# Optimization experiments

Measured on AMD Instinct MI355X. Metric: run time of the kernel, lower is better.

## Reference

```python
import jax, jax.numpy as jnp
import numpy as np

EPS = 1e-12  # torch F.normalize default eps (clamp_min)

def _l2norm(v, axis):
    n = jnp.sqrt(jnp.sum(v * v, axis=axis, keepdims=True))
    return v / jnp.maximum(n, EPS)

def setup_inputs() -> dict:
    key = jax.random.key(0)
    k1, k2, k3 = jax.random.split(key, 3)
    N, D, H, W, K = 64, 128, 64, 64, 32
    x = jax.random.normal(k1, (N, D, H, W), dtype=jnp.float32)
    conv_w = jax.random.normal(k2, (K, D), dtype=jnp.float32)  # 1x1 conv weight, no bias
    centroids = jax.random.uniform(k3, (K, D), dtype=jnp.float32)
    return {"x": x, "conv_w": conv_w, "centroids": centroids}

def reference(x, conv_w, centroids):
    N, D, H, W = x.shape
    K = conv_w.shape[0]
    # descriptor-wise L2 normalization over channel dim
    x = _l2norm(x, axis=1)
    xf = x.reshape(N, D, H * W)                      # [N, D, P]
    # 1x1 conv == per-pixel linear: [K,D] @ [N,D,P] -> [N,K,P]
    logits = jnp.einsum('kd,ndp->nkp', conv_w, xf)
    soft_assign = jax.nn.softmax(logits, axis=1)     # softmax over clusters
    # vlad[n,k,d] = sum_p a[n,k,p]*(x[n,d,p] - c[k,d])
    #            = (a @ x^T)[n,k,d] - (sum_p a)[n,k] * c[k,d]
    agg = jnp.einsum('nkp,ndp->nkd', soft_assign, xf)
    asum = jnp.sum(soft_assign, axis=2)              # [N, K]
    vlad = agg - asum[:, :, None] * centroids[None]  # [N, K, D]
    vlad = _l2norm(vlad, axis=2)                     # intra-normalization
    vlad = vlad.reshape(N, K * D)
    vlad = _l2norm(vlad, axis=1)                     # global L2 norm
    return vlad
```

## Files before the change

### kernel.cpp

```cpp
#include <hip/hip_runtime.h>
#include <math.h>

#define N_IMG 64
#define D_CH  128
#define P_PIX 4096
#define K_CL  32
#define S_SPL 8
#define P_BLK (P_PIX / S_SPL)
#define TP    32
#define N_TILE (P_BLK / TP)

typedef __attribute__((ext_vector_type(8))) short bf16x8;
typedef __attribute__((ext_vector_type(4))) float f32x4;

#define MFMA(a, b, c) __builtin_amdgcn_mfma_f32_16x16x32_bf16(a, b, c, 0, 0, 0)

#define BAR() do {                                            \
    asm volatile("s_waitcnt lgkmcnt(0)" ::: "memory");        \
    __builtin_amdgcn_s_barrier();                             \
} while (0)

static __device__ __forceinline__ void split4t(float a, float b, float c, float d,
                                               ushort4 &h, ushort4 &l) {
    unsigned ua = __float_as_uint(a), ub = __float_as_uint(b);
    unsigned uc = __float_as_uint(c), ud = __float_as_uint(d);
    h.x = (ushort)(ua >> 16); h.y = (ushort)(ub >> 16);
    h.z = (ushort)(uc >> 16); h.w = (ushort)(ud >> 16);
    float ra = a - __uint_as_float(ua & 0xffff0000u);
    float rb = b - __uint_as_float(ub & 0xffff0000u);
    float rc = c - __uint_as_float(uc & 0xffff0000u);
    float rd = d - __uint_as_float(ud & 0xffff0000u);
    l.x = (ushort)(__float_as_uint(ra) >> 16);
    l.y = (ushort)(__float_as_uint(rb) >> 16);
    l.z = (ushort)(__float_as_uint(rc) >> 16);
    l.w = (ushort)(__float_as_uint(rd) >> 16);
}

__global__ __launch_bounds__(256)
void netvlad_main(const float* __restrict__ x, const float* __restrict__ w,
                  float* __restrict__ aggp, float* __restrict__ asump)
{
    __shared__ __align__(16) ushort xTh[32 * 136], xTl[32 * 136];
    __shared__ __align__(16) ushort xDh[128 * 40], xDl[128 * 40];
    __shared__ __align__(16) ushort aph[32 * 40],  apl[32 * 40];
    __shared__ __align__(16) float  xch[4][64][4];
    __shared__ float pbuf[4][32];
    __shared__ float asw[4][16];

    const int tid = threadIdx.x;
    const int n   = blockIdx.x >> 3;
    const int ps  = blockIdx.x & 7;

    const int l   = tid & 63;
    const int wid = tid >> 6;
    const int q   = l >> 4;
    const int ln  = l & 15;
    const int mt  = wid >> 1;
    const int nt  = wid & 1;

    bf16x8 wh[4], wl[4];
    #pragma unroll
    for (int kk = 0; kk < 4; ++kk) {
        const float* wp = w + (nt * 16 + ln) * D_CH + kk * 32 + 8 * q;
        float4 wa = *(const float4*)wp;
        float4 wb = *(const float4*)(wp + 4);
        ushort4 h1, l1, h2, l2;
        split4t(wa.x, wa.y, wa.z, wa.w, h1, l1);
        split4t(wb.x, wb.y, wb.z, wb.w, h2, l2);
        wh[kk][0] = (short)h1.x; wh[kk][1] = (short)h1.y; wh[kk][2] = (short)h1.z; wh[kk][3] = (short)h1.w;
        wh[kk][4] = (short)h2.x; wh[kk][5] = (short)h2.y; wh[kk][6] = (short)h2.z; wh[kk][7] = (short)h2.w;
        wl[kk][0] = (short)l1.x; wl[kk][1] = (short)l1.y; wl[kk][2] = (short)l1.z; wl[kk][3] = (short)l1.w;
        wl[kk][4] = (short)l2.x; wl[kk][5] = (short)l2.y; wl[kk][6] = (short)l2.z; wl[kk][7] = (short)l2.w;
    }

    f32x4 acc2[2][2];
    #pragma unroll
    for (int a = 0; a < 2; ++a)
        #pragma unroll
        for (int b = 0; b < 2; ++b)
            acc2[a][b] = (f32x4){0.f, 0.f, 0.f, 0.f};
    float asacc = 0.0f;

    const float* xin = x + (size_t)n * D_CH * P_PIX + ps * P_BLK;

    const int pT    = tid & 31;
    const int dbase = (tid >> 5) * 16;

    float4 xv[4];
    float  tv[16];
    {
        const float* xt = xin;
        #pragma unroll
        for (int it = 0; it < 4; ++it) {
            int d = it * 32 + (tid >> 3);
            xv[it] = *(const float4*)(xt + d * P_PIX + 4 * (tid & 7));
        }
        #pragma unroll
        for (int j = 0; j < 16; ++j)
            tv[j] = xt[(size_t)(dbase + j) * P_PIX + pT];
    }

    for (int t = 0; t < N_TILE; ++t) {
        #pragma unroll
        for (int it = 0; it < 4; ++it) {
            int d = it * 32 + (tid >> 3);
            ushort4 h, lo;
            split4t(xv[it].x, xv[it].y, xv[it].z, xv[it].w, h, lo);
            *(ushort4*)&xDh[d * 40 + 4 * (tid & 7)] = h;
            *(ushort4*)&xDl[d * 40 + 4 * (tid & 7)] = lo;
        }

        float sq = 0.f;
        #pragma unroll
        for (int c = 0; c < 4; ++c) {
            ushort4 h, lo;
            split4t(tv[4*c+0], tv[4*c+1], tv[4*c+2], tv[4*c+3], h, lo);
            *(ushort4*)&xTh[pT * 136 + dbase + 4 * c] = h;
            *(ushort4*)&xTl[pT * 136 + dbase + 4 * c] = lo;
            sq += tv[4*c+0]*tv[4*c+0] + tv[4*c+1]*tv[4*c+1]
                + tv[4*c+2]*tv[4*c+2] + tv[4*c+3]*tv[4*c+3];
        }
        sq += __shfl_xor(sq, 32);
        if (l < 32) pbuf[wid][pT] = sq;

        if (t + 1 < N_TILE) {
            const float* xt2 = xin + (t + 1) * TP;
            #pragma unroll
            for (int it = 0; it < 4; ++it) {
                int d = it * 32 + (tid >> 3);
                xv[it] = *(const float4*)(xt2 + d * P_PIX + 4 * (tid & 7));
            }
            #pragma unroll
            for (int j = 0; j < 16; ++j)
                tv[j] = xt2[(size_t)(dbase + j) * P_PIX + pT];
        }
        BAR();

        float spx, spy, spz, spw;
        {
            int pp = l & 31;
            int jb = (l >> 5) * 2;
            float vsq = pbuf[jb][pp] + pbuf[jb + 1][pp];
            vsq += __shfl_xor(vsq, 32);
            float sSl = 1.0f / fmaxf(sqrtf(vsq), 1e-12f);
            int p0 = mt * 16 + 4 * q;
            spx = __shfl(sSl, p0 + 0);
            spy = __shfl(sSl, p0 + 1);
            spz = __shfl(sSl, p0 + 2);
            spw = __shfl(sSl, p0 + 3);
        }

        f32x4 acc1 = (f32x4){0.f, 0.f, 0.f, 0.f};
        #pragma unroll
        for (int kk = 0; kk < 4; ++kk) {
            int ia = (mt * 16 + ln) * 136 + kk * 32 + 8 * q;
            bf16x8 Ah = *(const bf16x8*)&xTh[ia];
            bf16x8 Al = *(const bf16x8*)&xTl[ia];
            acc1 = MFMA(Ah, wh[kk], acc1);
            acc1 = MFMA(Ah, wl[kk], acc1);
            acc1 = MFMA(Al, wh[kk], acc1);
        }

        float e[4], s[4];
        e[0] = __builtin_expf(acc1[0] * spx);
        e[1] = __builtin_expf(acc1[1] * spy);
        e[2] = __builtin_expf(acc1[2] * spz);
        e[3] = __builtin_expf(acc1[3] * spw);
        #pragma unroll
        for (int r = 0; r < 4; ++r) {
            s[r] = e[r];
            s[r] += __shfl_xor(s[r], 1);
            s[r] += __shfl_xor(s[r], 2);
            s[r] += __shfl_xor(s[r], 4);
            s[r] += __shfl_xor(s[r], 8);
        }
        *(float4*)&xch[wid][l][0] = make_float4(s[0], s[1], s[2], s[3]);
        BAR();
        {
            float4 po = *(const float4*)&xch[wid ^ 1][l][0];
            float rt[4];
            rt[0] = __builtin_amdgcn_rcpf(s[0] + po.x);
            rt[1] = __builtin_amdgcn_rcpf(s[1] + po.y);
            rt[2] = __builtin_amdgcn_rcpf(s[2] + po.z);
            rt[3] = __builtin_amdgcn_rcpf(s[3] + po.w);
            float sm[4], ap[4];
            #pragma unroll
            for (int r = 0; r < 4; ++r) sm[r] = e[r] * rt[r];
            asacc += sm[0] + sm[1] + sm[2] + sm[3];
            ap[0] = sm[0] * spx; ap[1] = sm[1] * spy;
            ap[2] = sm[2] * spz; ap[3] = sm[3] * spw;
            ushort4 h, lo;
            split4t(ap[0], ap[1], ap[2], ap[3], h, lo);
            int ib = (nt * 16 + ln) * 40 + mt * 16 + 4 * q;
            *(ushort4*)&aph[ib] = h;
            *(ushort4*)&apl[ib] = lo;
        }
        BAR();

        bf16x8 A2h[2], A2l[2], B2h[2], B2l[2];
        #pragma unroll
        for (int m2 = 0; m2 < 2; ++m2) {
            int ia = ((2 * wid + m2) * 16 + ln) * 40 + 8 * q;
            A2h[m2] = *(const bf16x8*)&xDh[ia];
            A2l[m2] = *(const bf16x8*)&xDl[ia];
        }
        #pragma unroll
        for (int n2 = 0; n2 < 2; ++n2) {
            int ib = (n2 * 16 + ln) * 40 + 8 * q;
            B2h[n2] = *(const bf16x8*)&aph[ib];
            B2l[n2] = *(const bf16x8*)&apl[ib];
        }
        #pragma unroll
        for (int m2 = 0; m2 < 2; ++m2)
            #pragma unroll
            for (int n2 = 0; n2 < 2; ++n2) {
                acc2[m2][n2] = MFMA(A2h[m2], B2h[n2], acc2[m2][n2]);
                acc2[m2][n2] = MFMA(A2h[m2], B2l[n2], acc2[m2][n2]);
                acc2[m2][n2] = MFMA(A2l[m2], B2h[n2], acc2[m2][n2]);
            }
        BAR();
    }

    const int base = ((n * S_SPL + ps) * K_CL) * D_CH;
    #pragma unroll
    for (int m2 = 0; m2 < 2; ++m2)
        #pragma unroll
        for (int n2 = 0; n2 < 2; ++n2) {
            int k = n2 * 16 + ln;
            #pragma unroll
            for (int r = 0; r < 4; ++r) {
                int d = (2 * wid + m2) * 16 + 4 * q + r;
                aggp[base + k * D_CH + d] = acc2[m2][n2][r];
            }
        }
    asacc += __shfl_xor(asacc, 16);
    asacc += __shfl_xor(asacc, 32);
    if (l < 16) asw[wid][l] = asacc;
    __syncthreads();
    if (tid < K_CL)
        asump[(n * S_SPL + ps) * K_CL + tid] =
            asw[tid >> 4][tid & 15] + asw[(tid >> 4) + 2][tid & 15];
}

__global__ __launch_bounds__(256)
void netvlad_finish(const float* __restrict__ aggp, const float* __restrict__ asump,
                    const float* __restrict__ cen, float* __restrict__ out)
{
    __shared__ float red[K_CL][8];
    __shared__ float gw[4];
    __shared__ float gss;
    const int tid = threadIdx.x;
    const int n = blockIdx.x;
    const int k = tid >> 3;
    const int d0 = (tid & 7) << 4;

    float v[16];
    #pragma unroll
    for (int i = 0; i < 16; ++i) v[i] = 0.0f;
    float as = 0.0f;
    for (int qq = 0; qq < S_SPL; ++qq) {
        const float* src = aggp + (((n * S_SPL + qq) * K_CL) + k) * D_CH + d0;
        #pragma unroll
        for (int c = 0; c < 4; ++c) {
            float4 t4 = *(const float4*)(src + (c << 2));
            v[4*c+0] += t4.x; v[4*c+1] += t4.y; v[4*c+2] += t4.z; v[4*c+3] += t4.w;
        }
        as += asump[(n * S_SPL + qq) * K_CL + k];
    }
    const float* cp = cen + k * D_CH + d0;
    float ssq = 0.0f;
    #pragma unroll
    for (int c = 0; c < 4; ++c) {
        float4 c4 = *(const float4*)(cp + (c << 2));
        v[4*c+0] -= as * c4.x;
        v[4*c+1] -= as * c4.y;
        v[4*c+2] -= as * c4.z;
        v[4*c+3] -= as * c4.w;
    }
    #pragma unroll
    for (int i = 0; i < 16; ++i) ssq += v[i] * v[i];
    red[k][tid & 7] = ssq;
    __syncthreads();
    float s2 = 0.0f;
    #pragma unroll
    for (int j = 0; j < 8; ++j) s2 += red[k][j];
    const float sc1 = 1.0f / fmaxf(sqrtf(s2), 1e-12f);
    #pragma unroll
    for (int i = 0; i < 16; ++i) v[i] *= sc1;
    float g = ssq * sc1 * sc1;
    #pragma unroll
    for (int off = 1; off < 64; off <<= 1) g += __shfl_xor(g, off);
    if ((tid & 63) == 0) gw[tid >> 6] = g;
    __syncthreads();
    if (tid == 0) gss = 1.0f / fmaxf(sqrtf(gw[0] + gw[1] + gw[2] + gw[3]), 1e-12f);
    __syncthreads();
    const float gsc = gss;
    float* op = out + (size_t)n * (K_CL * D_CH) + k * D_CH + d0;
    #pragma unroll
    for (int c = 0; c < 4; ++c) {
        *(float4*)(op + (c << 2)) =
            make_float4(v[4*c+0]*gsc, v[4*c+1]*gsc, v[4*c+2]*gsc, v[4*c+3]*gsc);
    }
}

extern "C" void kernel_launch(void* const* d_in, const int* in_sizes, int n_in,
                              void* d_out, int out_size, void* d_ws, size_t ws_size,
                              hipStream_t stream)
{
    const float* x   = (const float*)d_in[0];
    const float* w   = (const float*)d_in[1];
    const float* cen = (const float*)d_in[2];
    float* out = (float*)d_out;

    float* aggp  = (float*)d_ws;
    float* asump = aggp + (size_t)N_IMG * S_SPL * K_CL * D_CH;

    netvlad_main<<<N_IMG * S_SPL, 256, 0, stream>>>(x, w, aggp, asump);
    netvlad_finish<<<N_IMG, 256, 0, stream>>>(aggp, asump, cen, out);
}
```

Baseline: 52.47 us.

## Load MFMA operands directly from global memory and double pixel tile size

```diff
diff --git a/kernel.cpp b/kernel.cpp
--- a/kernel.cpp
+++ b/kernel.cpp
@@ -7,8 +7,9 @@
 #define K_CL  32
 #define S_SPL 8
 #define P_BLK (P_PIX / S_SPL)
-#define TP    32
+#define TP    64
 #define N_TILE (P_BLK / TP)
+#define APLD  72
 
 typedef __attribute__((ext_vector_type(8))) short bf16x8;
 typedef __attribute__((ext_vector_type(4))) float f32x4;
@@ -36,16 +37,22 @@
     l.w = (ushort)(__float_as_uint(rd) >> 16);
 }
 
+static __device__ __forceinline__ void split8f(const float f[8], bf16x8 &h, bf16x8 &l) {
+    #pragma unroll
+    for (int i = 0; i < 8; ++i) {
+        unsigned u = __float_as_uint(f[i]);
+        h[i] = (short)(u >> 16);
+        float r = f[i] - __uint_as_float(u & 0xffff0000u);
+        l[i] = (short)(__float_as_uint(r) >> 16);
+    }
+}
+
 __global__ __launch_bounds__(256)
 void netvlad_main(const float* __restrict__ x, const float* __restrict__ w,
                   float* __restrict__ aggp, float* __restrict__ asump)
 {
-    __shared__ __align__(16) ushort xTh[32 * 136], xTl[32 * 136];
-    __shared__ __align__(16) ushort xDh[128 * 40], xDl[128 * 40];
-    __shared__ __align__(16) ushort aph[32 * 40],  apl[32 * 40];
-    __shared__ __align__(16) float  xch[4][64][4];
-    __shared__ float pbuf[4][32];
-    __shared__ float asw[4][16];
+    __shared__ __align__(16) ushort aph[K_CL * APLD], apl[K_CL * APLD];
+    __shared__ float asw[4][32];
 
     const int tid = threadIdx.x;
     const int n   = blockIdx.x >> 3;
@@ -55,23 +62,18 @@
     const int wid = tid >> 6;
     const int q   = l >> 4;
     const int ln  = l & 15;
-    const int mt  = wid >> 1;
-    const int nt  = wid & 1;
-
-    bf16x8 wh[4], wl[4];
-    #pragma unroll
-    for (int kk = 0; kk < 4; ++kk) {
-        const float* wp = w + (nt * 16 + ln) * D_CH + kk * 32 + 8 * q;
-        float4 wa = *(const float4*)wp;
-        float4 wb = *(const float4*)(wp + 4);
-        ushort4 h1, l1, h2, l2;
-        split4t(wa.x, wa.y, wa.z, wa.w, h1, l1);
-        split4t(wb.x, wb.y, wb.z, wb.w, h2, l2);
-        wh[kk][0] = (short)h1.x; wh[kk][1] = (short)h1.y; wh[kk][2] = (short)h1.z; wh[kk][3] = (short)h1.w;
-        wh[kk][4] = (short)h2.x; wh[kk][5] = (short)h2.y; wh[kk][6] = (short)h2.z; wh[kk][7] = (short)h2.w;
-        wl[kk][0] = (short)l1.x; wl[kk][1] = (short)l1.y; wl[kk][2] = (short)l1.z; wl[kk][3] = (short)l1.w;
-        wl[kk][4] = (short)l2.x; wl[kk][5] = (short)l2.y; wl[kk][6] = (short)l2.z; wl[kk][7] = (short)l2.w;
-    }
+
+    bf16x8 wh[2][4], wl[2][4];
+    #pragma unroll
+    for (int n2 = 0; n2 < 2; ++n2)
+        #pragma unroll
+        for (int kk = 0; kk < 4; ++kk) {
+            const float* wp = w + (n2 * 16 + ln) * D_CH + kk * 32 + 8 * q;
+            float fv[8];
+            *(float4*)&fv[0] = *(const float4*)wp;
+            *(float4*)&fv[4] = *(const float4*)(wp + 4);
+            split8f(fv, wh[n2][kk], wl[n2][kk]);
+        }
 
     f32x4 acc2[2][2];
     #pragma unroll
@@ -79,145 +81,116 @@
         #pragma unroll
         for (int b = 0; b < 2; ++b)
             acc2[a][b] = (f32x4){0.f, 0.f, 0.f, 0.f};
-    float asacc = 0.0f;
+    float asacc0 = 0.0f, asacc1 = 0.0f;
 
     const float* xin = x + (size_t)n * D_CH * P_PIX + ps * P_BLK;
-
-    const int pT    = tid & 31;
-    const int dbase = (tid >> 5) * 16;
-
-    float4 xv[4];
-    float  tv[16];
-    {
-        const float* xt = xin;
-        #pragma unroll
-        for (int it = 0; it < 4; ++it) {
-            int d = it * 32 + (tid >> 3);
-            xv[it] = *(const float4*)(xt + d * P_PIX + 4 * (tid & 7));
-        }
-        #pragma unroll
-        for (int j = 0; j < 16; ++j)
-            tv[j] = xt[(size_t)(dbase + j) * P_PIX + pT];
-    }
+    const int base_p = wid * 16 + ln;
 
     for (int t = 0; t < N_TILE; ++t) {
-        #pragma unroll
-        for (int it = 0; it < 4; ++it) {
-            int d = it * 32 + (tid >> 3);
-            ushort4 h, lo;
-            split4t(xv[it].x, xv[it].y, xv[it].z, xv[it].w, h, lo);
-            *(ushort4*)&xDh[d * 40 + 4 * (tid & 7)] = h;
-            *(ushort4*)&xDl[d * 40 + 4 * (tid & 7)] = lo;
-        }
+        const float* xt = xin + t * TP;
+
+        float av[4][8];
+        #pragma unroll
+        for (int kk = 0; kk < 4; ++kk)
+            #pragma unroll
+            for (int j = 0; j < 8; ++j)
+                av[kk][j] = xt[(size_t)(kk * 32 + 8 * q + j) * P_PIX + base_p];
 
         float sq = 0.f;
         #pragma unroll
-        for (int c = 0; c < 4; ++c) {
-            ushort4 h, lo;
-            split4t(tv[4*c+0], tv[4*c+1], tv[4*c+2], tv[4*c+3], h, lo);
-            *(ushort4*)&xTh[pT * 136 + dbase + 4 * c] = h;
-            *(ushort4*)&xTl[pT * 136 + dbase + 4 * c] = lo;
-            sq += tv[4*c+0]*tv[4*c+0] + tv[4*c+1]*tv[4*c+1]
-                + tv[4*c+2]*tv[4*c+2] + tv[4*c+3]*tv[4*c+3];
-        }
+        for (int kk = 0; kk < 4; ++kk)
+            #pragma unroll
+            for (int j = 0; j < 8; ++j)
+                sq += av[kk][j] * av[kk][j];
+        sq += __shfl_xor(sq, 16);
         sq += __shfl_xor(sq, 32);
-        if (l < 32) pbuf[wid][pT] = sq;
-
-        if (t + 1 < N_TILE) {
-            const float* xt2 = xin + (t + 1) * TP;
-            #pragma unroll
-            for (int it = 0; it < 4; ++it) {
-                int d = it * 32 + (tid >> 3);
-                xv[it] = *(const float4*)(xt2 + d * P_PIX + 4 * (tid & 7));
-            }
-            #pragma unroll
-            for (int j = 0; j < 16; ++j)
-                tv[j] = xt2[(size_t)(dbase + j) * P_PIX + pT];
-        }
-        BAR();
-
-        float spx, spy, spz, spw;
-        {
-            int pp = l & 31;
-            int jb = (l >> 5) * 2;
-            float vsq = pbuf[jb][pp] + pbuf[jb + 1][pp];
-            vsq += __shfl_xor(vsq, 32);
-            float sSl = 1.0f / fmaxf(sqrtf(vsq), 1e-12f);
-            int p0 = mt * 16 + 4 * q;
-            spx = __shfl(sSl, p0 + 0);
-            spy = __shfl(sSl, p0 + 1);
-            spz = __shfl(sSl, p0 + 2);
-            spw = __shfl(sSl, p0 + 3);
-        }
-
-        f32x4 acc1 = (f32x4){0.f, 0.f, 0.f, 0.f};
+        const float sSl = 1.0f / fmaxf(sqrtf(sq), 1e-12f);
+
+        f32x4 acc1_0 = (f32x4){0.f, 0.f, 0.f, 0.f};
+        f32x4 acc1_1 = (f32x4){0.f, 0.f, 0.f, 0.f};
         #pragma unroll
         for (int kk = 0; kk < 4; ++kk) {
-            int ia = (mt * 16 + ln) * 136 + kk * 32 + 8 * q;
-            bf16x8 Ah = *(const bf16x8*)&xTh[ia];
-            bf16x8 Al = *(const bf16x8*)&xTl[ia];
-            acc1 = MFMA(Ah, wh[kk], acc1);
-            acc1 = MFMA(Ah, wl[kk], acc1);
-            acc1 = MFMA(Al, wh[kk], acc1);
-        }
-
-        float e[4], s[4];
-        e[0] = __builtin_expf(acc1[0] * spx);
-        e[1] = __builtin_expf(acc1[1] * spy);
-        e[2] = __builtin_expf(acc1[2] * spz);
-        e[3] = __builtin_expf(acc1[3] * spw);
+            bf16x8 Ah, Al;
+            split8f(av[kk], Ah, Al);
+            acc1_0 = MFMA(Ah, wh[0][kk], acc1_0);
+            acc1_0 = MFMA(Ah, wl[0][kk], acc1_0);
+            acc1_0 = MFMA(Al, wh[0][kk], acc1_0);
+            acc1_1 = MFMA(Ah, wh[1][kk], acc1_1);
+            acc1_1 = MFMA(Ah, wl[1][kk], acc1_1);
+            acc1_1 = MFMA(Al, wh[1][kk], acc1_1);
+        }
+
+        float sp[4];
+        #pragma unroll
+        for (int r = 0; r < 4; ++r) sp[r] = __shfl(sSl, 4 * q + r);
+
+        float e0[4], e1[4], s[4];
         #pragma unroll
         for (int r = 0; r < 4; ++r) {
-            s[r] = e[r];
+            e0[r] = __builtin_expf(acc1_0[r] * sp[r]);
+            e1[r] = __builtin_expf(acc1_1[r] * sp[r]);
+        }
+        #pragma unroll
+        for (int r = 0; r < 4; ++r) {
+            s[r] = e0[r] + e1[r];
             s[r] += __shfl_xor(s[r], 1);
             s[r] += __shfl_xor(s[r], 2);
             s[r] += __shfl_xor(s[r], 4);
             s[r] += __shfl_xor(s[r], 8);
         }
-        *(float4*)&xch[wid][l][0] = make_float4(s[0], s[1], s[2], s[3]);
+        float rt[4];
+        #pragma unroll
+        for (int r = 0; r < 4; ++r) rt[r] = __builtin_amdgcn_rcpf(s[r]);
+
+        {
+            float sm0[4], sm1[4];
+            #pragma unroll
+            for (int r = 0; r < 4; ++r) {
+                sm0[r] = e0[r] * rt[r];
+                sm1[r] = e1[r] * rt[r];
+            }
+            asacc0 += sm0[0] + sm0[1] + sm0[2] + sm0[3];
+            asacc1 += sm1[0] + sm1[1] + sm1[2] + sm1[3];
+            ushort4 h, lo;
+            split4t(sm0[0] * sp[0], sm0[1] * sp[1], sm0[2] * sp[2], sm0[3] * sp[3], h, lo);
+            int ib0 = ln * APLD + wid * 16 + 4 * q;
+            *(ushort4*)&aph[ib0] = h;
+            *(ushort4*)&apl[ib0] = lo;
+            split4t(sm1[0] * sp[0], sm1[1] * sp[1], sm1[2] * sp[2], sm1[3] * sp[3], h, lo);
+            int ib1 = (16 + ln) * APLD + wid * 16 + 4 * q;
+            *(ushort4*)&aph[ib1] = h;
+            *(ushort4*)&apl[ib1] = lo;
+        }
         BAR();
-        {
-            float4 po = *(const float4*)&xch[wid ^ 1][l][0];
-            float rt[4];
-            rt[0] = __builtin_amdgcn_rcpf(s[0] + po.x);
-            rt[1] = __builtin_amdgcn_rcpf(s[1] + po.y);
-            rt[2] = __builtin_amdgcn_rcpf(s[2] + po.z);
-            rt[3] = __builtin_amdgcn_rcpf(s[3] + po.w);
-            float sm[4], ap[4];
-            #pragma unroll
-            for (int r = 0; r < 4; ++r) sm[r] = e[r] * rt[r];
-            asacc += sm[0] + sm[1] + sm[2] + sm[3];
-            ap[0] = sm[0] * spx; ap[1] = sm[1] * spy;
-            ap[2] = sm[2] * spz; ap[3] = sm[3] * spw;
-            ushort4 h, lo;
-            split4t(ap[0], ap[1], ap[2], ap[3], h, lo);
-            int ib = (nt * 16 + ln) * 40 + mt * 16 + 4 * q;
-            *(ushort4*)&aph[ib] = h;
-            *(ushort4*)&apl[ib] = lo;
-        }
-        BAR();
-
-        bf16x8 A2h[2], A2l[2], B2h[2], B2l[2];
-        #pragma unroll
-        for (int m2 = 0; m2 < 2; ++m2) {
-            int ia = ((2 * wid + m2) * 16 + ln) * 40 + 8 * q;
-            A2h[m2] = *(const bf16x8*)&xDh[ia];
-            A2l[m2] = *(const bf16x8*)&xDl[ia];
-        }
-        #pragma unroll
-        for (int n2 = 0; n2 < 2; ++n2) {
-            int ib = (n2 * 16 + ln) * 40 + 8 * q;
-            B2h[n2] = *(const bf16x8*)&aph[ib];
-            B2l[n2] = *(const bf16x8*)&apl[ib];
-        }
-        #pragma unroll
-        for (int m2 = 0; m2 < 2; ++m2)
-            #pragma unroll
-            for (int n2 = 0; n2 < 2; ++n2) {
-                acc2[m2][n2] = MFMA(A2h[m2], B2h[n2], acc2[m2][n2]);
-                acc2[m2][n2] = MFMA(A2h[m2], B2l[n2], acc2[m2][n2]);
-                acc2[m2][n2] = MFMA(A2l[m2], B2h[n2], acc2[m2][n2]);
-            }
+
+        #pragma unroll
+        for (int pc = 0; pc < 2; ++pc) {
+            bf16x8 Bh0, Bl0, Bh1, Bl1;
+            {
+                int ib = ln * APLD + pc * 32 + 8 * q;
+                Bh0 = *(const bf16x8*)&aph[ib];
+                Bl0 = *(const bf16x8*)&apl[ib];
+                ib = (16 + ln) * APLD + pc * 32 + 8 * q;
+                Bh1 = *(const bf16x8*)&aph[ib];
+                Bl1 = *(const bf16x8*)&apl[ib];
+            }
+            #pragma unroll
+            for (int m2 = 0; m2 < 2; ++m2) {
+                const float* ag = xt + (size_t)((2 * wid + m2) * 16 + ln) * P_PIX
+                                     + pc * 32 + 8 * q;
+                float fv[8];
+                *(float4*)&fv[0] = *(const float4*)ag;
+                *(float4*)&fv[4] = *(const float4*)(ag + 4);
+                bf16x8 Ah, Al;
+                split8f(fv, Ah, Al);
+                acc2[m2][0] = MFMA(Ah, Bh0, acc2[m2][0]);
+                acc2[m2][0] = MFMA(Ah, Bl0, acc2[m2][0]);
+                acc2[m2][0] = MFMA(Al, Bh0, acc2[m2][0]);
+                acc2[m2][1] = MFMA(Ah, Bh1, acc2[m2][1]);
+                acc2[m2][1] = MFMA(Ah, Bl1, acc2[m2][1]);
+                acc2[m2][1] = MFMA(Al, Bh1, acc2[m2][1]);
+            }
+        }
         BAR();
     }
 
@@ -233,13 +206,15 @@
                 aggp[base + k * D_CH + d] = acc2[m2][n2][r];
             }
         }
-    asacc += __shfl_xor(asacc, 16);
-    asacc += __shfl_xor(asacc, 32);
-    if (l < 16) asw[wid][l] = asacc;
+    asacc0 += __shfl_xor(asacc0, 16);
+    asacc0 += __shfl_xor(asacc0, 32);
+    asacc1 += __shfl_xor(asacc1, 16);
+    asacc1 += __shfl_xor(asacc1, 32);
+    if (l < 32) asw[wid][l] = (l < 16) ? asacc0 : asacc1;
     __syncthreads();
     if (tid < K_CL)
         asump[(n * S_SPL + ps) * K_CL + tid] =
-            asw[tid >> 4][tid & 15] + asw[(tid >> 4) + 2][tid & 15];
+            asw[0][tid] + asw[1][tid] + asw[2][tid] + asw[3][tid];
 }
 
 __global__ __launch_bounds__(256)
```

Result: slower. 56.91 us (+8.5%).
